# Kernel optimization log

Hardware: AMD Instinct MI355X
Metric: run time of the kernel (lower is better)

## Reference

```python
import jax, jax.numpy as jnp
import numpy as np
from jax import lax

K = 3
PAD = 1

def setup_inputs() -> dict:
    key = jax.random.key(0)
    ks = jax.random.split(key, 5)
    B, C, H, W, O = 4, 128, 128, 128, 256
    x = jax.random.normal(ks[0], (B, C, H, W), dtype=jnp.float32)
    w_off = jax.random.normal(ks[1], (3 * K * K, C, K, K), dtype=jnp.float32) * 0.05
    b_off = jnp.zeros((3 * K * K,), dtype=jnp.float32)
    w_dw = jax.random.normal(ks[2], (C, 1, K, K), dtype=jnp.float32) * 0.2
    b_dw = jnp.zeros((C,), dtype=jnp.float32)
    w_pw = jax.random.normal(ks[3], (O, C), dtype=jnp.float32) * (1.0 / np.sqrt(C))
    b_pw = jnp.zeros((O,), dtype=jnp.float32)
    return {"x": x, "w_off": w_off, "b_off": b_off, "w_dw": w_dw,
            "b_dw": b_dw, "w_pw": w_pw, "b_pw": b_pw}

def _dcn_forward(x, w_off, b_off, w_dw, b_dw, w_pw, b_pw):
    B, C, H, W = x.shape
    K2 = K * K
    # offset/mask conv (stride 1, pad 1) -> [B, 3*K*K, H, W]
    om = lax.conv_general_dilated(
        x, w_off, window_strides=(1, 1), padding=[(PAD, PAD), (PAD, PAD)],
        dimension_numbers=("NCHW", "OIHW", "NCHW")) + b_off[None, :, None, None]
    off = om[:, : 2 * K2]                      # [B, 2*K2, H, W]
    mask = jax.nn.sigmoid(om[:, 2 * K2:])      # [B, K2, H, W]
    dy = off[:, 0::2]                          # [B, K2, H, W] (y offsets)
    dx = off[:, 1::2]                          # [B, K2, H, W] (x offsets)
    # base sampling grid per kernel tap
    ky, kx = jnp.meshgrid(jnp.arange(K), jnp.arange(K), indexing="ij")
    ky = (ky.reshape(-1) - PAD).astype(x.dtype)   # [K2]
    kx = (kx.reshape(-1) - PAD).astype(x.dtype)
    py = jnp.arange(H, dtype=x.dtype)[None, None, :, None] + ky[None, :, None, None] + dy
    px = jnp.arange(W, dtype=x.dtype)[None, None, None, :] + kx[None, :, None, None] + dx
    y0 = jnp.floor(py); x0 = jnp.floor(px)
    wy = py - y0;       wx = px - x0

    def gather(yc, xc):
        # yc, xc: [B, K2, H, W] float corner coords; zero outside bounds
        valid = ((yc >= 0) & (yc < H) & (xc >= 0) & (xc < W)).astype(x.dtype)
        yi = jnp.clip(yc, 0, H - 1).astype(jnp.int32)
        xi = jnp.clip(xc, 0, W - 1).astype(jnp.int32)
        idx = yi * W + xi                       # [B, K2, H, W]
        def per_b(xb, ib):
            # xb: [C, H, W]; ib: [K2, H, W] -> [C, K2, H, W]
            return jnp.take(xb.reshape(C, -1), ib.reshape(-1), axis=1).reshape(C, K2, H, W)
        v = jax.vmap(per_b)(x, idx)             # [B, C, K2, H, W]
        return v * valid[:, None]

    val = (gather(y0, x0) * ((1 - wy) * (1 - wx))[:, None]
           + gather(y0, x0 + 1) * ((1 - wy) * wx)[:, None]
           + gather(y0 + 1, x0) * (wy * (1 - wx))[:, None]
           + gather(y0 + 1, x0 + 1) * (wy * wx)[:, None])  # [B, C, K2, H, W]
    val = val * mask[:, None]
    # depthwise deformable conv: per-channel K2 weights
    wk = w_dw.reshape(C, K2)
    out = jnp.einsum("bckhw,ck->bchw", val, wk) + b_dw[None, :, None, None]
    # pointwise 1x1 conv
    out = jnp.einsum("bchw,oc->bohw", out, w_pw) + b_pw[None, :, None, None]
    return out

def reference(x, w_off, b_off, w_dw, b_dw, w_pw, b_pw):
    return _dcn_forward(x, w_off, b_off, w_dw, b_dw, w_pw, b_pw)
```

## Files before the change

### kernel.cpp

```cpp
#include <hip/hip_runtime.h>
#include <hip/hip_bf16.h>
#include <math.h>

#define BB 4
#define CC 128
#define HH 128
#define WW 128
#define OO 256
#define HWP 16384

typedef __attribute__((ext_vector_type(8))) _Float16 half8;
typedef __attribute__((ext_vector_type(2))) _Float16 half2t;
typedef __attribute__((ext_vector_type(4))) float floatx4;

__device__ inline half2t u2h2(unsigned int u) {
  union { unsigned int i; half2t h; } z; z.i = u; return z.h;
}
__device__ inline unsigned short f2h_bits(float f) {
  union { _Float16 h; unsigned short s; } z; z.h = (_Float16)f; return z.s;
}

__global__ __launch_bounds__(256) void k_transpose(const float* __restrict__ x,
                                                   const float* __restrict__ w_off,
                                                   const float* __restrict__ w_pw,
                                                   unsigned int* __restrict__ xh32,
                                                   _Float16* __restrict__ Ah,
                                                   _Float16* __restrict__ Apw) {
  int tid = threadIdx.x;
  if (blockIdx.z == 4) {
    int e = (blockIdx.x * 128 + blockIdx.y) * 256 + tid;
    if (e < 144 * 32 * 8) {
      int kblk = e >> 8;
      int o = (e >> 3) & 31;
      int j = e & 7;
      int k = kblk * 8 + j;
      int t = k >> 7, c = k & 127;
      float w = (o < 27) ? w_off[(o * CC + c) * 9 + t] : 0.0f;
      Ah[e] = (_Float16)w;
    }
    int e2 = e - 144 * 32 * 8;
    if (e2 >= 0 && e2 < 16 * 256 * 8) {
      int cblk = e2 >> 11;
      int o = (e2 >> 3) & 255;
      int j = e2 & 7;
      Apw[e2] = (_Float16)w_pw[o * CC + cblk * 8 + j];
    }
    return;
  }
  __shared__ float tile[64][65];
  int wt = blockIdx.x & 1;
  int ct = blockIdx.x >> 1;
  int h = blockIdx.y, b = blockIdx.z;
  int tw = tid & 63;
  int tc = tid >> 6;
#pragma unroll
  for (int i = 0; i < 16; i++) {
    int c = ct * 64 + i * 4 + tc;
    tile[i * 4 + tc][tw] = x[((b * CC + c) * HH + h) * WW + wt * 64 + tw];
  }
  __syncthreads();
  int cp = tid & 31;
  int wq = tid >> 5;
#pragma unroll
  for (int i = 0; i < 8; i++) {
    int wp = i * 8 + wq;
    int w = wt * 64 + wp;
    unsigned short h0 = f2h_bits(tile[cp * 2][wp]);
    unsigned short h1 = f2h_bits(tile[cp * 2 + 1][wp]);
    int idx2 = (((b * HH + h) * WW + w) * CC + ct * 64 + cp * 2) >> 1;
    xh32[idx2] = (unsigned int)h0 | ((unsigned int)h1 << 16);
  }
}

__global__ __launch_bounds__(256) void k_offconv_mfma(
    const _Float16* __restrict__ xh, const _Float16* __restrict__ Ah,
    const float* __restrict__ b_off, float* __restrict__ om) {
  int bid = blockIdx.x;
  int xcd = bid & 7, r = bid >> 3;
  int b = r >> 4;
  int h = xcd * 16 + (r & 15);
  int tid = threadIdx.x;
  int wv = tid >> 6, lane = tid & 63;
  int w0 = wv * 32;
  int n16 = lane & 15, quad = lane >> 4;

  floatx4 acc[2][2] = {};
  half8 zz = {};

  for (int t = 0; t < 9; t++) {
    int dy = t / 3 - 1, dx = t % 3 - 1;
    int hs = h + dy;
    bool hok = ((unsigned)hs < HH);
    int hsc = min(max(hs, 0), HH - 1);
    int wA = w0 + n16 + dx;
    int wB = wA + 16;
    bool okA = hok && ((unsigned)wA < WW);
    bool okB = hok && ((unsigned)wB < WW);
    int wAc = min(max(wA, 0), WW - 1);
    int wBc = min(max(wB, 0), WW - 1);
    size_t offA = (size_t)((b * HH + hsc) * WW + wAc) * CC + quad * 8;
    size_t offB = (size_t)((b * HH + hsc) * WW + wBc) * CC + quad * 8;
#pragma unroll
    for (int cs = 0; cs < 4; cs++) {
      int co = cs * 32;
      half8 bhA = *(const half8*)(xh + offA + co);
      half8 bhB = *(const half8*)(xh + offB + co);
      bhA = okA ? bhA : zz;
      bhB = okB ? bhB : zz;
      int kblk = t * 16 + cs * 4 + quad;
      const _Float16* pa = Ah + (size_t)kblk * 256 + n16 * 8;
      half8 a0 = *(const half8*)pa;
      half8 a1 = *(const half8*)(pa + 128);
      acc[0][0] = __builtin_amdgcn_mfma_f32_16x16x32_f16(a0, bhA, acc[0][0], 0, 0, 0);
      acc[1][0] = __builtin_amdgcn_mfma_f32_16x16x32_f16(a1, bhA, acc[1][0], 0, 0, 0);
      acc[0][1] = __builtin_amdgcn_mfma_f32_16x16x32_f16(a0, bhB, acc[0][1], 0, 0, 0);
      acc[1][1] = __builtin_amdgcn_mfma_f32_16x16x32_f16(a1, bhB, acc[1][1], 0, 0, 0);
    }
  }
  int nbase = (b << 14) + (h << 7);
#pragma unroll
  for (int mt = 0; mt < 2; mt++) {
#pragma unroll
    for (int reg = 0; reg < 4; reg++) {
      int o = mt * 16 + quad * 4 + reg;
      if (o < 27) {
        float bo = b_off[o];
#pragma unroll
        for (int nf = 0; nf < 2; nf++) {
          int w = w0 + nf * 16 + n16;
          om[((size_t)(nbase + w) << 5) + o] = acc[mt][nf][reg] + bo;
        }
      }
    }
  }
}

__global__ __launch_bounds__(256, 4) void k_sample(const unsigned short* __restrict__ xh,
                                                   const float* __restrict__ om,
                                                   const float* __restrict__ w_dw,
                                                   const float* __restrict__ b_dw,
                                                   unsigned short* __restrict__ out1h) {
  __shared__ int s_base[8][9], s_dxs[8][9], s_dys[8][9];
  __shared__ unsigned int s_wp[8][9][2];
  __shared__ float s_wk[9][128];
  int tid = threadIdx.x;
  int bid = blockIdx.x;
  int n0 = ((bid & 7) * 1024 + (bid >> 3)) * 8;

  for (int i = tid; i < 1152; i += 256) s_wk[i % 9][i / 9] = w_dw[i];

  if (tid < 72) {
    int pix = tid / 9, k = tid - pix * 9;
    int n = n0 + pix;
    int b = n >> 14, rem = n & 16383;
    int h = rem >> 7, w = rem & 127;
    const float* op = om + ((size_t)n << 5);
    float dy = op[2 * k];
    float dx = op[2 * k + 1];
    float mv = op[18 + k];
    mv = 1.0f / (1.0f + __expf(-mv));
    float py = (float)(h + k / 3 - 1) + dy;
    float px = (float)(w + k % 3 - 1) + dx;
    float y0f = floorf(py), x0f = floorf(px);
    float wy = py - y0f, wx = px - x0f;
    int y0 = (int)y0f, x0 = (int)x0f;
    int y1 = y0 + 1, x1 = x0 + 1;
    float v00 = (y0 >= 0 && y0 < HH && x0 >= 0 && x0 < WW) ? 1.f : 0.f;
    float v01 = (y0 >= 0 && y0 < HH && x1 >= 0 && x1 < WW) ? 1.f : 0.f;
    float v10 = (y1 >= 0 && y1 < HH && x0 >= 0 && x0 < WW) ? 1.f : 0.f;
    float v11 = (y1 >= 0 && y1 < HH && x1 >= 0 && x1 < WW) ? 1.f : 0.f;
    int y0c = min(max(y0, 0), HH - 1), y1c = min(max(y1, 0), HH - 1);
    int x0c = min(max(x0, 0), WW - 1), x1c = min(max(x1, 0), WW - 1);
    s_base[pix][k] = ((b * HH + y0c) * WW + x0c) * CC;
    s_dxs[pix][k] = (x1c - x0c) * CC;
    s_dys[pix][k] = (y1c - y0c) * WW * CC;
    float w00 = (1.f - wy) * (1.f - wx) * mv * v00;
    float w01 = (1.f - wy) * wx * mv * v01;
    float w10 = wy * (1.f - wx) * mv * v10;
    float w11 = wy * wx * mv * v11;
    s_wp[pix][k][0] = (unsigned int)f2h_bits(w00) | ((unsigned int)f2h_bits(w01) << 16);
    s_wp[pix][k][1] = (unsigned int)f2h_bits(w10) | ((unsigned int)f2h_bits(w11) << 16);
  }
  __syncthreads();
  int wv = tid >> 6, lane = tid & 63;
  int pix = wv * 2 + (lane >> 5);
  int cl = lane & 31;
  int c0 = cl * 4;
  int n = n0 + pix;

  float acc0 = 0.f, acc1 = 0.f, acc2v = 0.f, acc3 = 0.f;
#pragma unroll
  for (int k = 0; k < 9; k++) {
    int base = s_base[pix][k] + c0;
    int dxs = s_dxs[pix][k], dys = s_dys[pix][k];
    uint2 a00 = *(const uint2*)(xh + base);
    uint2 a01 = *(const uint2*)(xh + base + dxs);
    uint2 a10 = *(const uint2*)(xh + base + dys);
    uint2 a11 = *(const uint2*)(xh + base + dys + dxs);
    half2t wt = u2h2(s_wp[pix][k][0]);
    half2t wb = u2h2(s_wp[pix][k][1]);
    unsigned int t0 = __builtin_amdgcn_perm(a01.x, a00.x, 0x05040100u);
    unsigned int t1 = __builtin_amdgcn_perm(a01.x, a00.x, 0x07060302u);
    unsigned int t2 = __builtin_amdgcn_perm(a01.y, a00.y, 0x05040100u);
    unsigned int t3 = __builtin_amdgcn_perm(a01.y, a00.y, 0x07060302u);
    unsigned int b0 = __builtin_amdgcn_perm(a11.x, a10.x, 0x05040100u);
    unsigned int b1 = __builtin_amdgcn_perm(a11.x, a10.x, 0x07060302u);
    unsigned int b2 = __builtin_amdgcn_perm(a11.y, a10.y, 0x05040100u);
    unsigned int b3 = __builtin_amdgcn_perm(a11.y, a10.y, 0x07060302u);
    float v0 = __builtin_amdgcn_fdot2(u2h2(b0), wb, __builtin_amdgcn_fdot2(u2h2(t0), wt, 0.f, false), false);
    float v1 = __builtin_amdgcn_fdot2(u2h2(b1), wb, __builtin_amdgcn_fdot2(u2h2(t1), wt, 0.f, false), false);
    float v2 = __builtin_amdgcn_fdot2(u2h2(b2), wb, __builtin_amdgcn_fdot2(u2h2(t2), wt, 0.f, false), false);
    float v3 = __builtin_amdgcn_fdot2(u2h2(b3), wb, __builtin_amdgcn_fdot2(u2h2(t3), wt, 0.f, false), false);
    float4 wv4 = *(const float4*)&s_wk[k][c0];
    acc0 = fmaf(v0, wv4.x, acc0);
    acc1 = fmaf(v1, wv4.y, acc1);
    acc2v = fmaf(v2, wv4.z, acc2v);
    acc3 = fmaf(v3, wv4.w, acc3);
  }
  float4 bd = *(const float4*)(b_dw + c0);
  acc0 += bd.x; acc1 += bd.y; acc2v += bd.z; acc3 += bd.w;
  ushort4 ov;
  ov.x = f2h_bits(acc0);
  ov.y = f2h_bits(acc1);
  ov.z = f2h_bits(acc2v);
  ov.w = f2h_bits(acc3);
  *(ushort4*)(out1h + (size_t)n * CC + c0) = ov;
}

__global__ __launch_bounds__(256) void k_pw_mfma(const _Float16* __restrict__ Apw,
                                                 const _Float16* __restrict__ out1h,
                                                 const float* __restrict__ bpw,
                                                 float* __restrict__ out) {
  int bid = blockIdx.x;
  int n0 = ((bid & 7) * 128 + (bid >> 3)) * 64;
  int tid = threadIdx.x;
  int wv = tid >> 6, lane = tid & 63;
  int n16 = lane & 15, quad = lane >> 4;
  int obase = wv * 64;

  floatx4 acc[4][4] = {};
#pragma unroll
  for (int cs = 0; cs < 4; cs++) {
    half8 af[4], bf[4];
#pragma unroll
    for (int mf = 0; mf < 4; mf++) {
      const _Float16* pa = Apw + ((size_t)(cs * 4 + quad) * 256 + obase + mf * 16 + n16) * 8;
      af[mf] = *(const half8*)pa;
    }
#pragma unroll
    for (int nf = 0; nf < 4; nf++) {
      const _Float16* pb = out1h + (size_t)(n0 + nf * 16 + n16) * CC + cs * 32 + quad * 8;
      bf[nf] = *(const half8*)pb;
    }
#pragma unroll
    for (int mf = 0; mf < 4; mf++)
#pragma unroll
      for (int nf = 0; nf < 4; nf++)
        acc[mf][nf] = __builtin_amdgcn_mfma_f32_16x16x32_f16(af[mf], bf[nf], acc[mf][nf], 0, 0, 0);
  }
  int b = n0 >> 14;
#pragma unroll
  for (int mf = 0; mf < 4; mf++) {
#pragma unroll
    for (int reg = 0; reg < 4; reg++) {
      int o = obase + mf * 16 + quad * 4 + reg;
      float bo = bpw[o];
#pragma unroll
      for (int nf = 0; nf < 4; nf++) {
        int n = n0 + nf * 16 + n16;
        int hw = n & 16383;
        out[((size_t)(b * OO + o) << 14) + hw] = acc[mf][nf][reg] + bo;
      }
    }
  }
}

extern "C" void kernel_launch(void* const* d_in, const int* in_sizes, int n_in,
                              void* d_out, int out_size, void* d_ws, size_t ws_size,
                              hipStream_t stream) {
  const float* x     = (const float*)d_in[0];
  const float* w_off = (const float*)d_in[1];
  const float* b_off = (const float*)d_in[2];
  const float* w_dw  = (const float*)d_in[3];
  const float* b_dw  = (const float*)d_in[4];
  const float* w_pw  = (const float*)d_in[5];
  const float* b_pw  = (const float*)d_in[6];
  float* out = (float*)d_out;
  float* ws  = (float*)d_ws;

  _Float16* xh = (_Float16*)out;
  float* om = out + 4194304;

  _Float16* out1h = (_Float16*)ws;
  _Float16* Ah = (_Float16*)(ws + 4194304);
  _Float16* Apw = Ah + 36864;

  k_transpose<<<dim3(4, 128, 5), 256, 0, stream>>>(x, w_off, w_pw,
                                                   (unsigned int*)xh, Ah, Apw);
  k_offconv_mfma<<<512, 256, 0, stream>>>(xh, Ah, b_off, om);
  k_sample<<<8192, 256, 0, stream>>>((const unsigned short*)xh, om, w_dw, b_dw,
                                     (unsigned short*)out1h);
  k_pw_mfma<<<1024, 256, 0, stream>>>(Apw, out1h, b_pw, out);
}
```

Before: 187.7 us.

## Fuse offset conv and deformable sampling into one kernel via shared memory

Merges the offset/mask MFMA convolution and the bilinear sampling/depthwise kernel into a single kernel that handles 32 pixels per block. The offset conv is split along K across the four waves, reduced through shared memory, and the offsets stay in LDS instead of going through a global om buffer. Each thread then samples 4 pixels. This removes one launch and the global round trip for the offsets, at the cost of a split-K reduction, extra barriers and more registers per thread.

```diff
diff --git a/kernel.cpp b/kernel.cpp
--- a/kernel.cpp
+++ b/kernel.cpp
@@ -72,39 +72,53 @@
   }
 }
 
-__global__ __launch_bounds__(256) void k_offconv_mfma(
+__global__ __launch_bounds__(256, 4) void k_fused(
     const _Float16* __restrict__ xh, const _Float16* __restrict__ Ah,
-    const float* __restrict__ b_off, float* __restrict__ om) {
+    const float* __restrict__ b_off, const float* __restrict__ w_dw,
+    const float* __restrict__ b_dw, unsigned short* __restrict__ out1h) {
+  __shared__ union SM {
+    float part[4][32][34];
+    struct {
+      int s_base[32][9];
+      int s_dxs[32][9];
+      int s_dys[32][9];
+      unsigned int s_wp[32][9][2];
+      float s_wk[9][128];
+    } p2;
+  } sm;
+  __shared__ float om_s[32][28];
+
+  int tid = threadIdx.x;
   int bid = blockIdx.x;
-  int xcd = bid & 7, r = bid >> 3;
-  int b = r >> 4;
-  int h = xcd * 16 + (r & 15);
-  int tid = threadIdx.x;
+  int n0 = ((bid & 7) * 256 + (bid >> 3)) * 32;
+  int b = n0 >> 14;
+  int h0 = (n0 >> 7) & 127;
+  int wbase = n0 & 127;
+
   int wv = tid >> 6, lane = tid & 63;
-  int w0 = wv * 32;
   int n16 = lane & 15, quad = lane >> 4;
 
-  floatx4 acc[2][2] = {};
-  half8 zz = {};
-
-  for (int t = 0; t < 9; t++) {
-    int dy = t / 3 - 1, dx = t % 3 - 1;
-    int hs = h + dy;
-    bool hok = ((unsigned)hs < HH);
-    int hsc = min(max(hs, 0), HH - 1);
-    int wA = w0 + n16 + dx;
-    int wB = wA + 16;
-    bool okA = hok && ((unsigned)wA < WW);
-    bool okB = hok && ((unsigned)wB < WW);
-    int wAc = min(max(wA, 0), WW - 1);
-    int wBc = min(max(wB, 0), WW - 1);
-    size_t offA = (size_t)((b * HH + hsc) * WW + wAc) * CC + quad * 8;
-    size_t offB = (size_t)((b * HH + hsc) * WW + wBc) * CC + quad * 8;
-#pragma unroll
-    for (int cs = 0; cs < 4; cs++) {
-      int co = cs * 32;
-      half8 bhA = *(const half8*)(xh + offA + co);
-      half8 bhB = *(const half8*)(xh + offB + co);
+  {
+    floatx4 acc[2][2] = {};
+    half8 zz = {};
+#pragma unroll
+    for (int kidx = 0; kidx < 9; kidx++) {
+      int ki = wv * 9 + kidx;
+      int t = ki >> 2, cs = ki & 3;
+      int dy = t / 3 - 1, dx = t % 3 - 1;
+      int hs = h0 + dy;
+      bool hok = ((unsigned)hs < HH);
+      int hsc = min(max(hs, 0), HH - 1);
+      int wA = wbase + n16 + dx;
+      int wB = wA + 16;
+      bool okA = hok && ((unsigned)wA < WW);
+      bool okB = hok && ((unsigned)wB < WW);
+      int wAc = min(max(wA, 0), WW - 1);
+      int wBc = min(max(wB, 0), WW - 1);
+      size_t offA = (size_t)((b * HH + hsc) * WW + wAc) * CC + cs * 32 + quad * 8;
+      size_t offB = (size_t)((b * HH + hsc) * WW + wBc) * CC + cs * 32 + quad * 8;
+      half8 bhA = *(const half8*)(xh + offA);
+      half8 bhB = *(const half8*)(xh + offB);
       bhA = okA ? bhA : zz;
       bhB = okB ? bhB : zz;
       int kblk = t * 16 + cs * 4 + quad;
@@ -116,53 +130,37 @@
       acc[0][1] = __builtin_amdgcn_mfma_f32_16x16x32_f16(a0, bhB, acc[0][1], 0, 0, 0);
       acc[1][1] = __builtin_amdgcn_mfma_f32_16x16x32_f16(a1, bhB, acc[1][1], 0, 0, 0);
     }
-  }
-  int nbase = (b << 14) + (h << 7);
-#pragma unroll
-  for (int mt = 0; mt < 2; mt++) {
-#pragma unroll
-    for (int reg = 0; reg < 4; reg++) {
-      int o = mt * 16 + quad * 4 + reg;
-      if (o < 27) {
-        float bo = b_off[o];
-#pragma unroll
-        for (int nf = 0; nf < 2; nf++) {
-          int w = w0 + nf * 16 + n16;
-          om[((size_t)(nbase + w) << 5) + o] = acc[mt][nf][reg] + bo;
-        }
-      }
-    }
-  }
-}
-
-__global__ __launch_bounds__(256, 4) void k_sample(const unsigned short* __restrict__ xh,
-                                                   const float* __restrict__ om,
-                                                   const float* __restrict__ w_dw,
-                                                   const float* __restrict__ b_dw,
-                                                   unsigned short* __restrict__ out1h) {
-  __shared__ int s_base[8][9], s_dxs[8][9], s_dys[8][9];
-  __shared__ unsigned int s_wp[8][9][2];
-  __shared__ float s_wk[9][128];
-  int tid = threadIdx.x;
-  int bid = blockIdx.x;
-  int n0 = ((bid & 7) * 1024 + (bid >> 3)) * 8;
-
-  for (int i = tid; i < 1152; i += 256) s_wk[i % 9][i / 9] = w_dw[i];
-
-  if (tid < 72) {
-    int pix = tid / 9, k = tid - pix * 9;
-    int n = n0 + pix;
-    int b = n >> 14, rem = n & 16383;
-    int h = rem >> 7, w = rem & 127;
-    const float* op = om + ((size_t)n << 5);
-    float dy = op[2 * k];
-    float dx = op[2 * k + 1];
-    float mv = op[18 + k];
+#pragma unroll
+    for (int mt = 0; mt < 2; mt++)
+#pragma unroll
+      for (int reg = 0; reg < 4; reg++)
+#pragma unroll
+        for (int nf = 0; nf < 2; nf++)
+          sm.part[wv][mt * 16 + quad * 4 + reg][nf * 16 + n16] = acc[mt][nf][reg];
+  }
+  __syncthreads();
+
+#pragma unroll
+  for (int i = 0; i < 4; i++) {
+    int idx = tid + i * 256;
+    int o = idx >> 5, px = idx & 31;
+    float v = sm.part[0][o][px] + sm.part[1][o][px] + sm.part[2][o][px] + sm.part[3][o][px];
+    if (o < 27) om_s[px][o] = v + b_off[o];
+  }
+  __syncthreads();
+
+  for (int i = tid; i < 1152; i += 256) sm.p2.s_wk[i % 9][i / 9] = w_dw[i];
+  for (int it = tid; it < 288; it += 256) {
+    int px = it / 9, k = it - px * 9;
+    int w = wbase + px;
+    float dyv = om_s[px][2 * k];
+    float dxv = om_s[px][2 * k + 1];
+    float mv = om_s[px][18 + k];
     mv = 1.0f / (1.0f + __expf(-mv));
-    float py = (float)(h + k / 3 - 1) + dy;
-    float px = (float)(w + k % 3 - 1) + dx;
-    float y0f = floorf(py), x0f = floorf(px);
-    float wy = py - y0f, wx = px - x0f;
+    float py = (float)(h0 + k / 3 - 1) + dyv;
+    float pxf = (float)(w + k % 3 - 1) + dxv;
+    float y0f = floorf(py), x0f = floorf(pxf);
+    float wy = py - y0f, wx = pxf - x0f;
     int y0 = (int)y0f, x0 = (int)x0f;
     int y1 = y0 + 1, x1 = x0 + 1;
     float v00 = (y0 >= 0 && y0 < HH && x0 >= 0 && x0 < WW) ? 1.f : 0.f;
@@ -171,60 +169,72 @@
     float v11 = (y1 >= 0 && y1 < HH && x1 >= 0 && x1 < WW) ? 1.f : 0.f;
     int y0c = min(max(y0, 0), HH - 1), y1c = min(max(y1, 0), HH - 1);
     int x0c = min(max(x0, 0), WW - 1), x1c = min(max(x1, 0), WW - 1);
-    s_base[pix][k] = ((b * HH + y0c) * WW + x0c) * CC;
-    s_dxs[pix][k] = (x1c - x0c) * CC;
-    s_dys[pix][k] = (y1c - y0c) * WW * CC;
+    sm.p2.s_base[px][k] = ((b * HH + y0c) * WW + x0c) * CC;
+    sm.p2.s_dxs[px][k] = (x1c - x0c) * CC;
+    sm.p2.s_dys[px][k] = (y1c - y0c) * WW * CC;
     float w00 = (1.f - wy) * (1.f - wx) * mv * v00;
     float w01 = (1.f - wy) * wx * mv * v01;
     float w10 = wy * (1.f - wx) * mv * v10;
     float w11 = wy * wx * mv * v11;
-    s_wp[pix][k][0] = (unsigned int)f2h_bits(w00) | ((unsigned int)f2h_bits(w01) << 16);
-    s_wp[pix][k][1] = (unsigned int)f2h_bits(w10) | ((unsigned int)f2h_bits(w11) << 16);
+    sm.p2.s_wp[px][k][0] = (unsigned int)f2h_bits(w00) | ((unsigned int)f2h_bits(w01) << 16);
+    sm.p2.s_wp[px][k][1] = (unsigned int)f2h_bits(w10) | ((unsigned int)f2h_bits(w11) << 16);
   }
   __syncthreads();
-  int wv = tid >> 6, lane = tid & 63;
-  int pix = wv * 2 + (lane >> 5);
+
+  int pg = wv * 2 + (lane >> 5);
   int cl = lane & 31;
   int c0 = cl * 4;
-  int n = n0 + pix;
-
-  float acc0 = 0.f, acc1 = 0.f, acc2v = 0.f, acc3 = 0.f;
+  const unsigned short* xs = (const unsigned short*)xh;
+
+  float ac[4][4];
+#pragma unroll
+  for (int p = 0; p < 4; p++)
+#pragma unroll
+    for (int j = 0; j < 4; j++) ac[p][j] = 0.f;
+
 #pragma unroll
   for (int k = 0; k < 9; k++) {
-    int base = s_base[pix][k] + c0;
-    int dxs = s_dxs[pix][k], dys = s_dys[pix][k];
-    uint2 a00 = *(const uint2*)(xh + base);
-    uint2 a01 = *(const uint2*)(xh + base + dxs);
-    uint2 a10 = *(const uint2*)(xh + base + dys);
-    uint2 a11 = *(const uint2*)(xh + base + dys + dxs);
-    half2t wt = u2h2(s_wp[pix][k][0]);
-    half2t wb = u2h2(s_wp[pix][k][1]);
-    unsigned int t0 = __builtin_amdgcn_perm(a01.x, a00.x, 0x05040100u);
-    unsigned int t1 = __builtin_amdgcn_perm(a01.x, a00.x, 0x07060302u);
-    unsigned int t2 = __builtin_amdgcn_perm(a01.y, a00.y, 0x05040100u);
-    unsigned int t3 = __builtin_amdgcn_perm(a01.y, a00.y, 0x07060302u);
-    unsigned int b0 = __builtin_amdgcn_perm(a11.x, a10.x, 0x05040100u);
-    unsigned int b1 = __builtin_amdgcn_perm(a11.x, a10.x, 0x07060302u);
-    unsigned int b2 = __builtin_amdgcn_perm(a11.y, a10.y, 0x05040100u);
-    unsigned int b3 = __builtin_amdgcn_perm(a11.y, a10.y, 0x07060302u);
-    float v0 = __builtin_amdgcn_fdot2(u2h2(b0), wb, __builtin_amdgcn_fdot2(u2h2(t0), wt, 0.f, false), false);
-    float v1 = __builtin_amdgcn_fdot2(u2h2(b1), wb, __builtin_amdgcn_fdot2(u2h2(t1), wt, 0.f, false), false);
-    float v2 = __builtin_amdgcn_fdot2(u2h2(b2), wb, __builtin_amdgcn_fdot2(u2h2(t2), wt, 0.f, false), false);
-    float v3 = __builtin_amdgcn_fdot2(u2h2(b3), wb, __builtin_amdgcn_fdot2(u2h2(t3), wt, 0.f, false), false);
-    float4 wv4 = *(const float4*)&s_wk[k][c0];
-    acc0 = fmaf(v0, wv4.x, acc0);
-    acc1 = fmaf(v1, wv4.y, acc1);
-    acc2v = fmaf(v2, wv4.z, acc2v);
-    acc3 = fmaf(v3, wv4.w, acc3);
+    float4 wk4 = *(const float4*)&sm.p2.s_wk[k][c0];
+#pragma unroll
+    for (int p = 0; p < 4; p++) {
+      int pix = pg + p * 8;
+      int base = sm.p2.s_base[pix][k] + c0;
+      int dxs = sm.p2.s_dxs[pix][k], dys = sm.p2.s_dys[pix][k];
+      uint2 a00 = *(const uint2*)(xs + base);
+      uint2 a01 = *(const uint2*)(xs + base + dxs);
+      uint2 a10 = *(const uint2*)(xs + base + dys);
+      uint2 a11 = *(const uint2*)(xs + base + dys + dxs);
+      half2t wt = u2h2(sm.p2.s_wp[pix][k][0]);
+      half2t wb = u2h2(sm.p2.s_wp[pix][k][1]);
+      unsigned int t0 = __builtin_amdgcn_perm(a01.x, a00.x, 0x05040100u);
+      unsigned int t1 = __builtin_amdgcn_perm(a01.x, a00.x, 0x07060302u);
+      unsigned int t2 = __builtin_amdgcn_perm(a01.y, a00.y, 0x05040100u);
+      unsigned int t3 = __builtin_amdgcn_perm(a01.y, a00.y, 0x07060302u);
+      unsigned int b0 = __builtin_amdgcn_perm(a11.x, a10.x, 0x05040100u);
+      unsigned int b1 = __builtin_amdgcn_perm(a11.x, a10.x, 0x07060302u);
+      unsigned int b2 = __builtin_amdgcn_perm(a11.y, a10.y, 0x05040100u);
+      unsigned int b3 = __builtin_amdgcn_perm(a11.y, a10.y, 0x07060302u);
+      float v0 = __builtin_amdgcn_fdot2(u2h2(b0), wb, __builtin_amdgcn_fdot2(u2h2(t0), wt, 0.f, false), false);
+      float v1 = __builtin_amdgcn_fdot2(u2h2(b1), wb, __builtin_amdgcn_fdot2(u2h2(t1), wt, 0.f, false), false);
+      float v2 = __builtin_amdgcn_fdot2(u2h2(b2), wb, __builtin_amdgcn_fdot2(u2h2(t2), wt, 0.f, false), false);
+      float v3 = __builtin_amdgcn_fdot2(u2h2(b3), wb, __builtin_amdgcn_fdot2(u2h2(t3), wt, 0.f, false), false);
+      ac[p][0] = fmaf(v0, wk4.x, ac[p][0]);
+      ac[p][1] = fmaf(v1, wk4.y, ac[p][1]);
+      ac[p][2] = fmaf(v2, wk4.z, ac[p][2]);
+      ac[p][3] = fmaf(v3, wk4.w, ac[p][3]);
+    }
   }
   float4 bd = *(const float4*)(b_dw + c0);
-  acc0 += bd.x; acc1 += bd.y; acc2v += bd.z; acc3 += bd.w;
-  ushort4 ov;
-  ov.x = f2h_bits(acc0);
-  ov.y = f2h_bits(acc1);
-  ov.z = f2h_bits(acc2v);
-  ov.w = f2h_bits(acc3);
-  *(ushort4*)(out1h + (size_t)n * CC + c0) = ov;
+#pragma unroll
+  for (int p = 0; p < 4; p++) {
+    int n = n0 + pg + p * 8;
+    ushort4 ov;
+    ov.x = f2h_bits(ac[p][0] + bd.x);
+    ov.y = f2h_bits(ac[p][1] + bd.y);
+    ov.z = f2h_bits(ac[p][2] + bd.z);
+    ov.w = f2h_bits(ac[p][3] + bd.w);
+    *(ushort4*)(out1h + (size_t)n * CC + c0) = ov;
+  }
 }
 
 __global__ __launch_bounds__(256) void k_pw_mfma(const _Float16* __restrict__ Apw,
@@ -289,7 +299,6 @@
   float* ws  = (float*)d_ws;
 
   _Float16* xh = (_Float16*)out;
-  float* om = out + 4194304;
 
   _Float16* out1h = (_Float16*)ws;
   _Float16* Ah = (_Float16*)(ws + 4194304);
@@ -297,8 +306,7 @@
 
   k_transpose<<<dim3(4, 128, 5), 256, 0, stream>>>(x, w_off, w_pw,
                                                    (unsigned int*)xh, Ah, Apw);
-  k_offconv_mfma<<<512, 256, 0, stream>>>(xh, Ah, b_off, om);
-  k_sample<<<8192, 256, 0, stream>>>((const unsigned short*)xh, om, w_dw, b_dw,
-                                     (unsigned short*)out1h);
+  k_fused<<<2048, 256, 0, stream>>>(xh, Ah, b_off, w_dw, b_dw,
+                                    (unsigned short*)out1h);
   k_pw_mfma<<<1024, 256, 0, stream>>>(Apw, out1h, b_pw, out);
 }
```

Result: faster. 179.3 us (-4.5%).
